# Optimization experiments

Measured on AMD Instinct MI355X. Metric: run time of the kernel, lower is better.

## Reference

```python
import itertools
import jax, jax.numpy as jnp
import numpy as np

N = 6          # particles per spin channel -> 720 permutations
D = 3          # spatial dim
HID = 64
BATCH = 2048


def _perms_and_signs(n):
    """All n! permutations in lexicographic order + their signs (+1/-1)."""
    perms = np.array(list(itertools.permutations(range(n))), dtype=np.int32)
    i, j = np.triu_indices(n, 1)
    inversions = (perms[:, i] > perms[:, j]).sum(axis=1)
    signs = np.where(inversions % 2 == 0, 1.0, -1.0).astype(np.float32)
    return jnp.asarray(perms), jnp.asarray(signs)


def setup_inputs() -> dict:
    key = jax.random.key(0)
    ks = jax.random.split(key, 6)
    scale1 = 1.0 / np.sqrt(N * D)
    scale2 = 1.0 / np.sqrt(HID)
    return {
        "x1": jax.random.normal(ks[0], (BATCH, N, D), dtype=jnp.float32),
        "x2": jax.random.normal(ks[1], (BATCH, N, D), dtype=jnp.float32),
        "W1a": jax.random.normal(ks[2], (N * D, HID), dtype=jnp.float32) * scale1,
        "b1a": jnp.zeros((HID,), dtype=jnp.float32),
        "W2a": jax.random.normal(ks[3], (HID, 1), dtype=jnp.float32) * scale2,
        "b2a": jnp.zeros((1,), dtype=jnp.float32),
        "W1b": jax.random.normal(ks[4], (N * D, HID), dtype=jnp.float32) * scale1,
        "b1b": jnp.zeros((HID,), dtype=jnp.float32),
        "W2b": jax.random.normal(ks[5], (HID, 1), dtype=jnp.float32) * scale2,
        "b2b": jnp.zeros((1,), dtype=jnp.float32),
    }


def _antisymmetrized_leaf(x, W1, b1, W2, b2):
    # x: (B, n, d). Gather all n! permutations along axis -2.
    n, d = x.shape[-2], x.shape[-1]
    perms, signs = _perms_and_signs(n)          # (n!, n), (n!,)
    x_perm = jnp.take(x, perms, axis=-2)        # (B, n!, n, d)
    x_perm = x_perm.reshape(x_perm.shape[:-2] + (n * d,))  # (B, n!, n*d)
    # fn_to_antisymmetrize: MLP (..., n*d) -> (..., 1)
    h = jnp.tanh(x_perm @ W1 + b1)              # (B, n!, HID)
    perms_out = h @ W2 + b2                     # (B, n!, 1)
    signed = signs[:, None] * perms_out         # (B, n!, 1)
    return jnp.sum(signed, axis=(-1, -2))       # (B,)


def reference(x1, x2, W1a, b1a, W2a, b2a, W1b, b1b, W2b, b2b):
    psi1 = _antisymmetrized_leaf(x1, W1a, b1a, W2a, b2a)
    psi2 = _antisymmetrized_leaf(x2, W1b, b1b, W2b, b2b)
    # logabs=True: sum_i log|psi_i|
    return jnp.log(jnp.abs(psi1)) + jnp.log(jnp.abs(psi2))
```

## Files before the change

kernel.cpp:

```cpp
#include <hip/hip_runtime.h>
#include <math.h>


__device__ __forceinline__ float fexp2(float x) {
#if __has_builtin(__builtin_amdgcn_exp2f)
    return __builtin_amdgcn_exp2f(x);
#else
    return exp2f(x);
#endif
}
__device__ __forceinline__ float frcp(float x) {
#if __has_builtin(__builtin_amdgcn_rcpf)
    return __builtin_amdgcn_rcpf(x);
#else
    return 1.0f / x;
#endif
}

constexpr int lowest_free(unsigned used) {
    for (int j = 0; j < 6; ++j)
        if (!(used & (1u << j))) return j;
    return -1;
}

struct Tbl {
    float F[6][4];
    float w[6][6];
    float s[6][6];
    float q[6][6];
};

template <int LVL, unsigned USED, int PAR>
struct Node {
    template <int J>
    static __device__ __forceinline__ void step(const Tbl& T, float P,
                                                double& a0, double& a1) {
        if constexpr ((USED & (1u << J)) == 0) {
            constexpr int par2 = PAR ^ (__builtin_popcount(USED >> (J + 1)) & 1);
            if constexpr (LVL == 0)
                Node<1, (1u << J), par2>::go(T, T.F[J][0], a0, a1);
            else
                Node<LVL + 1, USED | (1u << J), par2>::go(T, P * T.F[J][LVL], a0, a1);
        }
    }
    static __device__ __forceinline__ void go(const Tbl& T, float P,
                                              double& a0, double& a1) {
        step<0>(T, P, a0, a1);
        step<1>(T, P, a0, a1);
        step<2>(T, P, a0, a1);
        step<3>(T, P, a0, a1);
        step<4>(T, P, a0, a1);
        step<5>(T, P, a0, a1);
    }
};

template <unsigned USED, int PAR>
struct Node<3, USED, PAR> {
    template <int X, int A, int B>
    static __device__ __forceinline__ float child_den(const Tbl& T, float P3,
                                                      float& n) {
        float P4 = P3 * T.F[X][3];
        float Q  = P4 * P4;
        n = P4 * T.w[A][B];
        return fmaf(Q, T.q[A][B], fmaf(P4, T.s[A][B], 1.0f));
    }
    template <int X, int A, int B>
    static constexpr int child_sign() {
        constexpr unsigned U4 = USED | (1u << X);
        constexpr int inv_x = __builtin_popcount(USED >> (X + 1));
        constexpr int inv_a = __builtin_popcount(U4 >> (A + 1));
        constexpr int inv_b = __builtin_popcount((U4 | (1u << A)) >> (B + 1));
        return (PAR ^ ((inv_x + inv_a + inv_b) & 1));
    }
    static __device__ __forceinline__ void go(const Tbl& T, float P3,
                                              double& a0, double& a1) {
        constexpr int x0 = lowest_free(USED);
        constexpr int x1 = lowest_free(USED | (1u << x0));
        constexpr int x2 = lowest_free(USED | (1u << x0) | (1u << x1));
        constexpr float sg0 = child_sign<x0, x1, x2>() ? -1.0f : 1.0f;
        constexpr float sg1 = child_sign<x1, x0, x2>() ? -1.0f : 1.0f;
        constexpr float sg2 = child_sign<x2, x0, x1>() ? -1.0f : 1.0f;

        float n0, n1, n2;
        float den0 = child_den<x0, x1, x2>(T, P3, n0);
        float den1 = child_den<x1, x0, x2>(T, P3, n1);
        float den2 = child_den<x2, x0, x1>(T, P3, n2);

        float d01 = den0 * den1;
        float den = d01 * den2;
        float t01 = (sg0 * n0) * den1 + (sg1 * n1) * den0;
        float num = t01 * den2 + (sg2 * n2) * d01;
        float r = num * frcp(den);
        if constexpr (USED & 1) a1 += (double)r;
        else                    a0 += (double)r;
    }
};

__global__ __launch_bounds__(256, 2) void antisym_kernel(
    const float* __restrict__ x1, const float* __restrict__ x2,
    const float* __restrict__ W1a, const float* __restrict__ b1a,
    const float* __restrict__ W2a,
    const float* __restrict__ W1b, const float* __restrict__ b1b,
    const float* __restrict__ W2b,
    float* __restrict__ out, int B) {
    __shared__ float lds_log[4];

    const int lane = threadIdx.x & 63;
    const int wave = threadIdx.x >> 6;
    const int ch = wave & 1;

    const float* W1 = ch ? W1b : W1a;
    const float* b1 = ch ? b1b : b1a;
    const float* W2 = ch ? W2b : W2a;
    const float* x  = ch ? x2  : x1;

    const float K = 2.8853900817779268f;
    float w1c[18];
#pragma unroll
    for (int r = 0; r < 18; ++r) w1c[r] = W1[r * 64 + lane] * K;
    const float b1s = b1[lane] * K;
    const float w2v = W2[lane];

#pragma unroll
    for (int it = 0; it < 2; ++it) {
        const int b = blockIdx.x * 4 + it * 2 + (wave >> 1);
        if (b < B) {
            float xv[18];
            const float* xb = x + b * 18;
#pragma unroll
            for (int r = 0; r < 18; ++r) xv[r] = xb[r];

            Tbl T;
            float F4[6], F5[6], g[6];
#pragma unroll
            for (int j = 0; j < 6; ++j) {
#pragma unroll
                for (int i = 0; i < 6; ++i) {
                    float c = xv[j * 3 + 0] * w1c[i * 3 + 0] +
                              xv[j * 3 + 1] * w1c[i * 3 + 1] +
                              xv[j * 3 + 2] * w1c[i * 3 + 2];
                    if (i == 0) c += b1s;
                    float e = fexp2(c);
                    if (i < 4) T.F[j][i] = e;
                    else if (i == 4) F4[j] = e;
                    else F5[j] = e;
                }
                g[j] = F4[j] * F5[j];
            }
#pragma unroll
            for (int a = 0; a < 6; ++a)
#pragma unroll
                for (int bb = a + 1; bb < 6; ++bb) {
                    float u = F4[a] * F5[bb];
                    float v = F4[bb] * F5[a];
                    T.w[a][bb] = v - u;
                    T.s[a][bb] = u + v;
                    T.q[a][bb] = g[a] * g[bb];
                }

            double acc0 = 0.0, acc1 = 0.0;
            Node<0, 0u, 0>::go(T, 1.0f, acc0, acc1);

            double v = (double)w2v * (acc0 + acc1) * -2.0;
#pragma unroll
            for (int off = 32; off > 0; off >>= 1) v += __shfl_xor(v, off, 64);

            if (lane == 0) lds_log[wave] = logf(fabsf((float)v));
        }
        __syncthreads();
        if (threadIdx.x < 2) {
            int bb = blockIdx.x * 4 + it * 2 + threadIdx.x;
            if (bb < B)
                out[bb] = lds_log[threadIdx.x * 2] + lds_log[threadIdx.x * 2 + 1];
        }
        __syncthreads();
    }
}

extern "C" void kernel_launch(void* const* d_in, const int* in_sizes, int n_in,
                              void* d_out, int out_size, void* d_ws, size_t ws_size,
                              hipStream_t stream) {
    const float* x1  = (const float*)d_in[0];
    const float* x2  = (const float*)d_in[1];
    const float* W1a = (const float*)d_in[2];
    const float* b1a = (const float*)d_in[3];
    const float* W2a = (const float*)d_in[4];
    const float* W1b = (const float*)d_in[6];
    const float* b1b = (const float*)d_in[7];
    const float* W2b = (const float*)d_in[8];

    const int B = in_sizes[0] / 18;
    float* out = (float*)d_out;

    dim3 grid((B + 3) / 4), block(256);
    hipLaunchKernelGGL(antisym_kernel, grid, block, 0, stream,
                       x1, x2, W1a, b1a, W2a, W1b, b1b, W2b, out, B);
}
```

Before: 97.19 us.

## Process two batch elements per wave with packed float2 math

Each wave now evaluates two batch elements together, holding every table entry and intermediate as a 2-wide float vector so the compiler can emit packed FP32 ops (v_pk_mul/v_pk_fma) on CDNA. The old loop over two iterations with two block barriers becomes a single pass with one barrier, and the double accumulators become 2-wide. The aim is to roughly halve the VALU instruction count for the permutation tree and amortise the per-lane weight loads. The cost is doubled register pressure for the tables, which could cause spills or lower occupancy under the 256x2 launch bound.

```diff
diff --git a/kernel.cpp b/kernel.cpp
--- a/kernel.cpp
+++ b/kernel.cpp
@@ -1,6 +1,9 @@
 #include <hip/hip_runtime.h>
 #include <math.h>
 
+
+typedef float  v2f __attribute__((ext_vector_type(2)));
+typedef double v2d __attribute__((ext_vector_type(2)));
 
 __device__ __forceinline__ float fexp2(float x) {
 #if __has_builtin(__builtin_amdgcn_exp2f)
@@ -16,6 +19,12 @@
     return 1.0f / x;
 #endif
 }
+__device__ __forceinline__ v2f vrcp(v2f v) {
+    v2f r; r.x = frcp(v.x); r.y = frcp(v.y); return r;
+}
+__device__ __forceinline__ v2f vfma(v2f a, v2f b, v2f c) {
+    return __builtin_elementwise_fma(a, b, c);
+}
 
 constexpr int lowest_free(unsigned used) {
     for (int j = 0; j < 6; ++j)
@@ -24,17 +33,17 @@
 }
 
 struct Tbl {
-    float F[6][4];
-    float w[6][6];
-    float s[6][6];
-    float q[6][6];
+    v2f F[6][4];
+    v2f w[6][6];
+    v2f s[6][6];
+    v2f q[6][6];
 };
 
 template <int LVL, unsigned USED, int PAR>
 struct Node {
     template <int J>
-    static __device__ __forceinline__ void step(const Tbl& T, float P,
-                                                double& a0, double& a1) {
+    static __device__ __forceinline__ void step(const Tbl& T, v2f P,
+                                                v2d& a0, v2d& a1) {
         if constexpr ((USED & (1u << J)) == 0) {
             constexpr int par2 = PAR ^ (__builtin_popcount(USED >> (J + 1)) & 1);
             if constexpr (LVL == 0)
@@ -43,8 +52,8 @@
                 Node<LVL + 1, USED | (1u << J), par2>::go(T, P * T.F[J][LVL], a0, a1);
         }
     }
-    static __device__ __forceinline__ void go(const Tbl& T, float P,
-                                              double& a0, double& a1) {
+    static __device__ __forceinline__ void go(const Tbl& T, v2f P,
+                                              v2d& a0, v2d& a1) {
         step<0>(T, P, a0, a1);
         step<1>(T, P, a0, a1);
         step<2>(T, P, a0, a1);
@@ -57,12 +66,13 @@
 template <unsigned USED, int PAR>
 struct Node<3, USED, PAR> {
     template <int X, int A, int B>
-    static __device__ __forceinline__ float child_den(const Tbl& T, float P3,
-                                                      float& n) {
-        float P4 = P3 * T.F[X][3];
-        float Q  = P4 * P4;
+    static __device__ __forceinline__ v2f child_den(const Tbl& T, v2f P3,
+                                                    v2f& n) {
+        v2f P4 = P3 * T.F[X][3];
+        v2f Q  = P4 * P4;
         n = P4 * T.w[A][B];
-        return fmaf(Q, T.q[A][B], fmaf(P4, T.s[A][B], 1.0f));
+        v2f one; one.x = 1.0f; one.y = 1.0f;
+        return vfma(Q, T.q[A][B], vfma(P4, T.s[A][B], one));
     }
     template <int X, int A, int B>
     static constexpr int child_sign() {
@@ -72,27 +82,29 @@
         constexpr int inv_b = __builtin_popcount((U4 | (1u << A)) >> (B + 1));
         return (PAR ^ ((inv_x + inv_a + inv_b) & 1));
     }
-    static __device__ __forceinline__ void go(const Tbl& T, float P3,
-                                              double& a0, double& a1) {
+    static __device__ __forceinline__ void go(const Tbl& T, v2f P3,
+                                              v2d& a0, v2d& a1) {
         constexpr int x0 = lowest_free(USED);
         constexpr int x1 = lowest_free(USED | (1u << x0));
         constexpr int x2 = lowest_free(USED | (1u << x0) | (1u << x1));
-        constexpr float sg0 = child_sign<x0, x1, x2>() ? -1.0f : 1.0f;
-        constexpr float sg1 = child_sign<x1, x0, x2>() ? -1.0f : 1.0f;
-        constexpr float sg2 = child_sign<x2, x0, x1>() ? -1.0f : 1.0f;
-
-        float n0, n1, n2;
-        float den0 = child_den<x0, x1, x2>(T, P3, n0);
-        float den1 = child_den<x1, x0, x2>(T, P3, n1);
-        float den2 = child_den<x2, x0, x1>(T, P3, n2);
-
-        float d01 = den0 * den1;
-        float den = d01 * den2;
-        float t01 = (sg0 * n0) * den1 + (sg1 * n1) * den0;
-        float num = t01 * den2 + (sg2 * n2) * d01;
-        float r = num * frcp(den);
-        if constexpr (USED & 1) a1 += (double)r;
-        else                    a0 += (double)r;
+
+        v2f n0, n1, n2;
+        v2f den0 = child_den<x0, x1, x2>(T, P3, n0);
+        v2f den1 = child_den<x1, x0, x2>(T, P3, n1);
+        v2f den2 = child_den<x2, x0, x1>(T, P3, n2);
+
+        v2f n0s = child_sign<x0, x1, x2>() ? -n0 : n0;
+        v2f n1s = child_sign<x1, x0, x2>() ? -n1 : n1;
+        v2f n2s = child_sign<x2, x0, x1>() ? -n2 : n2;
+
+        v2f d01 = den0 * den1;
+        v2f den = d01 * den2;
+        v2f t01 = vfma(n0s, den1, n1s * den0);
+        v2f num = vfma(t01, den2, n2s * d01);
+        v2f r = num * vrcp(den);
+        v2d rd = __builtin_convertvector(r, v2d);
+        if constexpr (USED & 1) a1 += rd;
+        else                    a0 += rd;
     }
 };
 
@@ -103,77 +115,89 @@
     const float* __restrict__ W1b, const float* __restrict__ b1b,
     const float* __restrict__ W2b,
     float* __restrict__ out, int B) {
-    __shared__ float lds_log[4];
+    __shared__ float lds_log[8];
 
     const int lane = threadIdx.x & 63;
     const int wave = threadIdx.x >> 6;
+    const int pi = wave >> 1;
     const int ch = wave & 1;
 
+    const float* x  = ch ? x2  : x1;
     const float* W1 = ch ? W1b : W1a;
     const float* b1 = ch ? b1b : b1a;
     const float* W2 = ch ? W2b : W2a;
-    const float* x  = ch ? x2  : x1;
-
-    const float K = 2.8853900817779268f;
-    float w1c[18];
-#pragma unroll
-    for (int r = 0; r < 18; ++r) w1c[r] = W1[r * 64 + lane] * K;
-    const float b1s = b1[lane] * K;
-    const float w2v = W2[lane];
-
-#pragma unroll
-    for (int it = 0; it < 2; ++it) {
-        const int b = blockIdx.x * 4 + it * 2 + (wave >> 1);
-        if (b < B) {
-            float xv[18];
-            const float* xb = x + b * 18;
-#pragma unroll
-            for (int r = 0; r < 18; ++r) xv[r] = xb[r];
-
-            Tbl T;
-            float F4[6], F5[6], g[6];
-#pragma unroll
-            for (int j = 0; j < 6; ++j) {
-#pragma unroll
-                for (int i = 0; i < 6; ++i) {
-                    float c = xv[j * 3 + 0] * w1c[i * 3 + 0] +
-                              xv[j * 3 + 1] * w1c[i * 3 + 1] +
-                              xv[j * 3 + 2] * w1c[i * 3 + 2];
-                    if (i == 0) c += b1s;
-                    float e = fexp2(c);
-                    if (i < 4) T.F[j][i] = e;
-                    else if (i == 4) F4[j] = e;
-                    else F5[j] = e;
-                }
-                g[j] = F4[j] * F5[j];
+
+    const int b0 = blockIdx.x * 4 + pi * 2;
+    const int b1i = b0 + 1;
+    const int b1c = (b1i < B) ? b1i : (B - 1);
+
+    if (b0 < B) {
+        const float K = 2.8853900817779268f;
+
+        float w1c[18];
+#pragma unroll
+        for (int r = 0; r < 18; ++r) w1c[r] = W1[r * 64 + lane] * K;
+        const float b1s = b1[lane] * K;
+        const float w2v = W2[lane];
+
+        v2f xv[18];
+        const float* xa = x + b0 * 18;
+        const float* xb = x + b1c * 18;
+#pragma unroll
+        for (int r = 0; r < 18; ++r) { xv[r].x = xa[r]; xv[r].y = xb[r]; }
+
+        Tbl T;
+        v2f F4[6], F5[6], g[6];
+#pragma unroll
+        for (int j = 0; j < 6; ++j) {
+#pragma unroll
+            for (int i = 0; i < 6; ++i) {
+                v2f c = xv[j * 3 + 0] * w1c[i * 3 + 0] +
+                        xv[j * 3 + 1] * w1c[i * 3 + 1] +
+                        xv[j * 3 + 2] * w1c[i * 3 + 2];
+                if (i == 0) { c.x += b1s; c.y += b1s; }
+                v2f e; e.x = fexp2(c.x); e.y = fexp2(c.y);
+                if (i < 4) T.F[j][i] = e;
+                else if (i == 4) F4[j] = e;
+                else F5[j] = e;
             }
-#pragma unroll
-            for (int a = 0; a < 6; ++a)
-#pragma unroll
-                for (int bb = a + 1; bb < 6; ++bb) {
-                    float u = F4[a] * F5[bb];
-                    float v = F4[bb] * F5[a];
-                    T.w[a][bb] = v - u;
-                    T.s[a][bb] = u + v;
-                    T.q[a][bb] = g[a] * g[bb];
-                }
-
-            double acc0 = 0.0, acc1 = 0.0;
-            Node<0, 0u, 0>::go(T, 1.0f, acc0, acc1);
-
-            double v = (double)w2v * (acc0 + acc1) * -2.0;
-#pragma unroll
-            for (int off = 32; off > 0; off >>= 1) v += __shfl_xor(v, off, 64);
-
-            if (lane == 0) lds_log[wave] = logf(fabsf((float)v));
-        }
-        __syncthreads();
-        if (threadIdx.x < 2) {
-            int bb = blockIdx.x * 4 + it * 2 + threadIdx.x;
-            if (bb < B)
-                out[bb] = lds_log[threadIdx.x * 2] + lds_log[threadIdx.x * 2 + 1];
-        }
-        __syncthreads();
+            g[j] = F4[j] * F5[j];
+        }
+#pragma unroll
+        for (int a = 0; a < 6; ++a)
+#pragma unroll
+            for (int bb = a + 1; bb < 6; ++bb) {
+                v2f u = F4[a] * F5[bb];
+                v2f v = F4[bb] * F5[a];
+                T.w[a][bb] = v - u;
+                T.s[a][bb] = u + v;
+                T.q[a][bb] = g[a] * g[bb];
+            }
+
+        v2d acc0; acc0.x = 0.0; acc0.y = 0.0;
+        v2d acc1; acc1.x = 0.0; acc1.y = 0.0;
+        v2f one; one.x = 1.0f; one.y = 1.0f;
+        Node<0, 0u, 0>::go(T, one, acc0, acc1);
+
+        double v0 = (double)w2v * (acc0.x + acc1.x) * -2.0;
+        double v1 = (double)w2v * (acc0.y + acc1.y) * -2.0;
+#pragma unroll
+        for (int off = 32; off > 0; off >>= 1) {
+            v0 += __shfl_xor(v0, off, 64);
+            v1 += __shfl_xor(v1, off, 64);
+        }
+
+        if (lane == 0) {
+            lds_log[(pi * 2 + 0) * 2 + ch] = logf(fabsf((float)v0));
+            if (b1i < B)
+                lds_log[(pi * 2 + 1) * 2 + ch] = logf(fabsf((float)v1));
+        }
+    }
+    __syncthreads();
+    if (threadIdx.x < 4) {
+        int bb = blockIdx.x * 4 + threadIdx.x;
+        if (bb < B)
+            out[bb] = lds_log[threadIdx.x * 2 + 0] + lds_log[threadIdx.x * 2 + 1];
     }
 }
 
```

After: 87.47 us. -10.0%, faster.
